# Performance work log

Measured on AMD Instinct MI355X. Metric: run time of the kernel, lower is better.

## Reference

```python
import jax, jax.numpy as jnp
import numpy as np

N_GROUPS = 32  # getGroupSize(.) assumed -> channels // 8 (or //24 for 3*ch) == 32 for ch=256
HEADS = 4


def group_norm(x, gamma, beta, groups=N_GROUPS, eps=1e-5):
    n, c = x.shape
    xg = x.reshape(n, groups, c // groups)
    mu = xg.mean(-1, keepdims=True)
    var = xg.var(-1, keepdims=True)
    xn = ((xg - mu) * jax.lax.rsqrt(var + eps)).reshape(n, c)
    return xn * gamma + beta


def setup_inputs():
    key = jax.random.key(0)
    N, E, CH, HID = 2000, 16000, 256, 256
    ks = jax.random.split(key, 24)

    def w(k, shape, s=0.02):
        return (jax.random.normal(k, shape) * s).astype(jnp.float32)

    inp = {
        'x': jax.random.normal(ks[0], (N, CH), jnp.float32),
        'edge_index': jax.random.randint(ks[1], (2, E), 0, N),
        'edge_attr': jax.random.normal(ks[2], (E, CH), jnp.float32),
        # edge_mlp: GN(3ch)+ReLU -> Linear(3ch,hid) -> GN(hid)+ReLU -> Linear(hid,ch)
        'gn_e1_g': jnp.ones((3 * CH,), jnp.float32), 'gn_e1_b': jnp.zeros((3 * CH,), jnp.float32),
        'We1': w(ks[3], (3 * CH, HID)), 'be1': jnp.zeros((HID,), jnp.float32),
        'gn_e2_g': jnp.ones((HID,), jnp.float32), 'gn_e2_b': jnp.zeros((HID,), jnp.float32),
        'We2': w(ks[4], (HID, CH)), 'be2': jnp.zeros((CH,), jnp.float32),
        # actN: GN(ch)+ReLU
        'gn_n_g': jnp.ones((CH,), jnp.float32), 'gn_n_b': jnp.zeros((CH,), jnp.float32),
        # multi-head attention projections
        'Wq': w(ks[5], (CH, CH)), 'bq': jnp.zeros((CH,), jnp.float32),
        'Wk': w(ks[6], (CH, CH)), 'bk': jnp.zeros((CH,), jnp.float32),
        'Wv': w(ks[7], (CH, CH)), 'bv': jnp.zeros((CH,), jnp.float32),
        'Wo': w(ks[8], (CH, CH)), 'bo': jnp.zeros((CH,), jnp.float32),
        # node_mlp: Linear(2ch,hid) -> GN(hid)+ReLU -> Linear(hid,ch)
        'Wn1': w(ks[9], (2 * CH, HID)), 'bn1': jnp.zeros((HID,), jnp.float32),
        'gn_n2_g': jnp.ones((HID,), jnp.float32), 'gn_n2_b': jnp.zeros((HID,), jnp.float32),
        'Wn2': w(ks[10], (HID, CH)), 'bn2': jnp.zeros((CH,), jnp.float32),
    }
    return inp


def reference(x, edge_index, edge_attr,
              gn_e1_g, gn_e1_b, We1, be1, gn_e2_g, gn_e2_b, We2, be2,
              gn_n_g, gn_n_b, Wq, bq, Wk, bk, Wv, bv, Wo, bo,
              Wn1, bn1, gn_n2_g, gn_n2_b, Wn2, bn2):
    row, col = edge_index[0], edge_index[1]
    N, ch = x.shape
    E = edge_attr.shape[0]
    dk = ch // HEADS

    # ---- edge model: cat(src, tgt, e) -> GN/ReLU -> Lin -> GN/ReLU -> Lin (+res) ----
    e_in = jnp.concatenate([x[row], x[col], edge_attr], axis=1)  # [E, 3ch]
    h = jax.nn.relu(group_norm(e_in, gn_e1_g, gn_e1_b))
    h = h @ We1 + be1
    h = jax.nn.relu(group_norm(h, gn_e2_g, gn_e2_b))
    e_out = h @ We2 + be2 + edge_attr  # [E, ch]

    # ---- node model: dense-masked MHA, queries=nodes, keys/values=edges ----
    mask = jnp.zeros((N, E), x.dtype).at[col, jnp.arange(E)].set(1.0)  # scatter adjacency
    q = (x @ Wq + bq).reshape(N, HEADS, dk)
    k = (e_out @ Wk + bk).reshape(E, HEADS, dk)
    v = (e_out @ Wv + bv).reshape(E, HEADS, dk)
    scores = jnp.einsum('nhd,ehd->hne', q, k) / jnp.sqrt(jnp.float32(dk))  # [H, N, E]
    scores = jnp.where(mask[None] > 0, scores, jnp.float32(-1e9))
    attn = jax.nn.softmax(scores, axis=-1)
    g = jnp.einsum('hne,ehd->nhd', attn, v).reshape(N, ch) @ Wo + bo  # [N, ch]

    xa = jax.nn.relu(group_norm(x, gn_n_g, gn_n_b))
    h = jnp.concatenate([xa, g], axis=1) @ Wn1 + bn1  # thinker='cat'
    h = jax.nn.relu(group_norm(h, gn_n2_g, gn_n2_b))
    n_out = h @ Wn2 + bn2 + x  # residual

    return n_out, e_out
```

## Files before the change

kernel.cpp:

```cpp
#include <hip/hip_runtime.h>
#include <hip/hip_bf16.h>
#include <stdint.h>
#include <math.h>

#define CH 256

typedef __attribute__((ext_vector_type(8)))  short short8;
typedef __attribute__((ext_vector_type(16))) short short16;
typedef __attribute__((ext_vector_type(4)))  float f32x4;

#define GL2LDS16(g, l) __builtin_amdgcn_global_load_lds(                       \
    (const __attribute__((address_space(1))) void*)(g),                        \
    (__attribute__((address_space(3))) void*)(l), 16, 0, 0)

__device__ inline short f2bf(float f) {
    __hip_bfloat16 h = __float2bfloat16(f);
    short s;
    __builtin_memcpy(&s, &h, 2);
    return s;
}

__device__ inline float bf2f(short s) {
    unsigned u = ((unsigned)(unsigned short)s) << 16;
    float f;
    __builtin_memcpy(&f, &u, 4);
    return f;
}

__device__ inline float warp_sum64(float v) {
    v += __shfl_xor(v, 32, 64);
    v += __shfl_xor(v, 16, 64);
    v += __shfl_xor(v, 8, 64);
    v += __shfl_xor(v, 4, 64);
    v += __shfl_xor(v, 2, 64);
    v += __shfl_xor(v, 1, 64);
    return v;
}

__device__ inline float warp_max64(float v) {
    v = fmaxf(v, __shfl_xor(v, 32, 64));
    v = fmaxf(v, __shfl_xor(v, 16, 64));
    v = fmaxf(v, __shfl_xor(v, 8, 64));
    v = fmaxf(v, __shfl_xor(v, 4, 64));
    v = fmaxf(v, __shfl_xor(v, 2, 64));
    v = fmaxf(v, __shfl_xor(v, 1, 64));
    return v;
}

struct GArgs {
    const short* A; const short* Bt; const float* bias; const float* res;
    float* C; short* Cbf;
    const float* gamma; const float* beta; float* vbar;
    int M, K, Nc, ldc, coff;
    const short* A2; const short* Bt2; const float* bias2; short* Cbf2;
    int M2, Nc2, y_split;
    const short* xbf; const short* eabf; const int* rowi; const int* coli;
    const float* mu; const float* rs; const float* vg; const float* vbt;
    int* cursor; int* elist;
};

template <int BM, int BN, int AMODE, int EPI, int DUAL, int VB, int FILL>
__global__ __launch_bounds__(256) void mfma_gemm(GArgs g)
{
    constexpr int BK = 64;
    constexpr int AK = AMODE ? (BK + 8) : BK;
    constexpr int HM = BM / 2, HN = BN / 2;
    constexpr int FM = HM / 16, FN = HN / 16;
    constexpr int PA = BM / 32;
    constexpr int PB = BN / 32;
    __shared__ short As[BM * AK];
    __shared__ short Bs[BN * BK];
    __shared__ int sidx[AMODE ? 2 * BM : 1];

    const short* A = g.A; const short* Bt = g.Bt;
    const float* bias = g.bias; const float* res = g.res;
    float* C = g.C; short* Cbf = g.Cbf;
    int M = g.M, ldc = g.ldc, co = g.coff;
    const int K = g.K;
    int by = blockIdx.y, bx = blockIdx.x;
    bool qrole = false;
    if constexpr (DUAL) {
        if (by >= g.y_split) {
            by -= g.y_split;
            if (bx * BN >= g.Nc2) return;
            qrole = true;
            A = g.A2; Bt = g.Bt2; bias = g.bias2; Cbf = g.Cbf2;
            C = nullptr; res = nullptr;
            M = g.M2; ldc = g.Nc2; co = 0;
        }
    }

    const int t = threadIdx.x;
    const int wave = t >> 6, lane = t & 63;
    const int q = lane >> 4, l16 = lane & 15;
    const int row0 = by * BM;
    const int col0 = bx * BN;
    const int wm = wave & 1, wn = wave >> 1;

    if constexpr (AMODE) {
        if (t < BM) {
            int gr = row0 + t; if (gr >= M) gr = M - 1;
            sidx[t] = g.rowi[gr];
            sidx[BM + t] = g.coli[gr];
        }
        __syncthreads();
    }

    if constexpr (FILL) {
        if (!qrole && bx == 0 && t < BM) {
            int rg = row0 + t;
            if (rg < M) {
                int c = g.coli[rg];
                int p = atomicAdd(&g.cursor[c], 1);
                g.elist[p] = rg;
            }
        }
    }

    f32x4 acc[FM][FN];
    #pragma unroll
    for (int i = 0; i < FM; i++)
        #pragma unroll
        for (int j = 0; j < FN; j++) acc[i][j] = (f32x4){0.f, 0.f, 0.f, 0.f};

    for (int k0 = 0; k0 < K; k0 += BK) {
        if constexpr (AMODE == 1) {
            int reg = k0 >> 8;
            int rloc = t >> 3;
            int c8 = (t & 7) * 8;
            int pos = k0 + c8;
            int G = pos / 24;
            float4 ga  = *(const float4*)&g.vg[pos];
            float4 ga2 = *(const float4*)&g.vg[pos + 4];
            float4 gb  = *(const float4*)&g.vbt[pos];
            float4 gb2 = *(const float4*)&g.vbt[pos + 4];
            int off = pos & 255;
            #pragma unroll
            for (int p = 0; p < BM / 32; p++) {
                int r2 = p * 32 + rloc;
                int e = row0 + r2; if (e >= M) e = M - 1;
                const short* srow;
                if (reg == 0)      srow = g.xbf + (size_t)sidx[r2] * CH;
                else if (reg == 1) srow = g.xbf + (size_t)sidx[BM + r2] * CH;
                else               srow = g.eabf + (size_t)e * CH;
                short8 v8 = *(const short8*)&srow[off];
                float mm = g.mu[(size_t)e * 32 + G];
                float rr = g.rs[(size_t)e * 32 + G];
                short8 o;
                o[0] = f2bf(fmaxf((bf2f(v8[0]) - mm) * rr * ga.x + gb.x, 0.f));
                o[1] = f2bf(fmaxf((bf2f(v8[1]) - mm) * rr * ga.y + gb.y, 0.f));
                o[2] = f2bf(fmaxf((bf2f(v8[2]) - mm) * rr * ga.z + gb.z, 0.f));
                o[3] = f2bf(fmaxf((bf2f(v8[3]) - mm) * rr * ga.w + gb.w, 0.f));
                o[4] = f2bf(fmaxf((bf2f(v8[4]) - mm) * rr * ga2.x + gb2.x, 0.f));
                o[5] = f2bf(fmaxf((bf2f(v8[5]) - mm) * rr * ga2.y + gb2.y, 0.f));
                o[6] = f2bf(fmaxf((bf2f(v8[6]) - mm) * rr * ga2.z + gb2.z, 0.f));
                o[7] = f2bf(fmaxf((bf2f(v8[7]) - mm) * rr * ga2.w + gb2.w, 0.f));
                *(short8*)&As[r2 * AK + c8] = o;
            }
        } else {
            #pragma unroll
            for (int p = 0; p < PA; p++) {
                int chunk = p * 256 + t;
                int r = chunk >> 3;
                int cs = (((chunk & 7) ^ (r & 7)) * 8);
                int gr = row0 + r; if (gr >= M) gr = M - 1;
                const short* gsrc = A + (size_t)gr * K + k0 + cs;
                short* ldst = &As[(p * 256 + wave * 64) * 8];
                GL2LDS16(gsrc, ldst);
            }
        }
        #pragma unroll
        for (int p = 0; p < PB; p++) {
            int chunk = p * 256 + t;
            int r = chunk >> 3;
            int cs = (((chunk & 7) ^ (r & 7)) * 8);
            const short* gsrc = Bt + (size_t)(col0 + r) * K + k0 + cs;
            short* ldst = &Bs[(p * 256 + wave * 64) * 8];
            GL2LDS16(gsrc, ldst);
        }
        __syncthreads();
        #pragma unroll
        for (int ks = 0; ks < 2; ks++) {
            short8 af[FM], bf[FN];
            #pragma unroll
            for (int mi = 0; mi < FM; mi++) {
                int R = wm * HM + mi * 16 + l16;
                if constexpr (AMODE == 1)
                    af[mi] = *(const short8*)&As[R * AK + ks * 32 + q * 8];
                else {
                    int slot = ((ks * 4 + q) ^ (R & 7)) * 8;
                    af[mi] = *(const short8*)&As[R * BK + slot];
                }
            }
            #pragma unroll
            for (int ni = 0; ni < FN; ni++) {
                int R = wn * HN + ni * 16 + l16;
                int slot = ((ks * 4 + q) ^ (R & 7)) * 8;
                bf[ni] = *(const short8*)&Bs[R * BK + slot];
            }
            #pragma unroll
            for (int mi = 0; mi < FM; mi++)
                #pragma unroll
                for (int ni = 0; ni < FN; ni++)
                    acc[mi][ni] = __builtin_amdgcn_mfma_f32_16x16x32_bf16(
                        af[mi], bf[ni], acc[mi][ni], 0, 0, 0);
        }
        __syncthreads();
    }

    #pragma unroll
    for (int ni = 0; ni < FN; ni++) {
        int cg = col0 + wn * HN + ni * 16 + l16;
        float bv = bias[cg];
        if constexpr (EPI == 1) {
            float ga = g.gamma[cg], be = g.beta[cg];
            #pragma unroll
            for (int mi = 0; mi < FM; mi++) {
                #pragma unroll
                for (int r = 0; r < 4; r++) {
                    float v = acc[mi][ni][r] + bv;
                    float s = v, sq = v * v;
                    s += __shfl_xor(s, 1, 64);  sq += __shfl_xor(sq, 1, 64);
                    s += __shfl_xor(s, 2, 64);  sq += __shfl_xor(sq, 2, 64);
                    s += __shfl_xor(s, 4, 64);  sq += __shfl_xor(sq, 4, 64);
                    float mean = s * 0.125f;
                    float var = sq * 0.125f - mean * mean;
                    float o = fmaxf((v - mean) * rsqrtf(var + 1e-5f) * ga + be, 0.f);
                    int rg = row0 + wm * HM + mi * 16 + q * 4 + r;
                    if (rg < M) Cbf[(size_t)rg * ldc + co + cg] = f2bf(o);
                }
            }
        } else {
            #pragma unroll
            for (int mi = 0; mi < FM; mi++) {
                #pragma unroll
                for (int r = 0; r < 4; r++) {
                    int rg = row0 + wm * HM + mi * 16 + q * 4 + r;
                    if (rg < M) {
                        float v = acc[mi][ni][r] + bv;
                        if (res) v += res[(size_t)rg * ldc + co + cg];
                        if (C)   C[(size_t)rg * ldc + co + cg] = v;
                        if (Cbf) Cbf[(size_t)rg * ldc + co + cg] = f2bf(v);
                    }
                }
            }
            if constexpr (VB) {
                if (!qrole && cg >= 256) {
                    float part = 0.f;
                    #pragma unroll
                    for (int mi = 0; mi < FM; mi++)
                        #pragma unroll
                        for (int r = 0; r < 4; r++) {
                            int rg = row0 + wm * HM + mi * 16 + q * 4 + r;
                            if (rg < M) part += acc[mi][ni][r] + bv;
                        }
                    part += __shfl_xor(part, 16, 64);
                    part += __shfl_xor(part, 32, 64);
                    if (q == 0) atomicAdd(&g.vbar[cg - 256], part);
                }
            }
        }
    }
}

struct PrepPack {
    const float* wsrc[8];
    short* wdst[8];
    int wK[8];
    int wstart[8];
    int NW, NP;
    const float* x;
    short* x_bf;
    short* cat_bf;
    float2* xs;
    const float* gng;
    const float* gnb;
    float* vbar;
    const float* bk;
    const float* bv;
    float* bkv;
    int* counts;
    int N;
};

__global__ __launch_bounds__(256) void prep_kernel(PrepPack p)
{
    int bid = blockIdx.x;
    int t = threadIdx.x;
    if (bid < p.NW) {
        int m = 0;
        #pragma unroll
        for (int i = 1; i < 8; i++) if (bid >= p.wstart[i]) m = i;
        int k0 = (bid - p.wstart[m]) * 16;
        const float* src = p.wsrc[m];
        short16 o;
        #pragma unroll
        for (int j = 0; j < 16; j++) o[j] = f2bf(src[(size_t)(k0 + j) * 256 + t]);
        *(short16*)(p.wdst[m] + (size_t)t * p.wK[m] + k0) = o;
        return;
    }
    if (bid >= p.NW + p.NP) {
        int i = (bid - p.NW - p.NP) * 256 + t;
        if (i < p.N) p.counts[i] = 0;
        return;
    }
    int pb = bid - p.NW;
    if (pb == 0) {
        p.vbar[t] = 0.f;
        p.bkv[t] = p.bk[t];
        p.bkv[256 + t] = p.bv[t];
    }
    int r = pb * 8 + (t >> 5);
    int g = t & 31;
    if (r >= p.N) return;
    size_t xb = (size_t)r * CH + g * 8;
    float4 a = *(const float4*)&p.x[xb];
    float4 b = *(const float4*)&p.x[xb + 4];
    short8 xr;
    xr[0] = f2bf(a.x); xr[1] = f2bf(a.y); xr[2] = f2bf(a.z); xr[3] = f2bf(a.w);
    xr[4] = f2bf(b.x); xr[5] = f2bf(b.y); xr[6] = f2bf(b.z); xr[7] = f2bf(b.w);
    *(short8*)&p.x_bf[xb] = xr;
    float s  = a.x + a.y + a.z + a.w + b.x + b.y + b.z + b.w;
    float s2 = a.x*a.x + a.y*a.y + a.z*a.z + a.w*a.w
             + b.x*b.x + b.y*b.y + b.z*b.z + b.w*b.w;
    p.xs[(size_t)r * 32 + g] = make_float2(s, s2);
    float m = s * 0.125f;
    float var = s2 * 0.125f - m * m;
    float rsd = rsqrtf(var + 1e-5f);
    float4 g0 = *(const float4*)&p.gng[g * 8];
    float4 g1 = *(const float4*)&p.gng[g * 8 + 4];
    float4 b0 = *(const float4*)&p.gnb[g * 8];
    float4 b1 = *(const float4*)&p.gnb[g * 8 + 4];
    short8 o;
    o[0] = f2bf(fmaxf((a.x - m) * rsd * g0.x + b0.x, 0.f));
    o[1] = f2bf(fmaxf((a.y - m) * rsd * g0.y + b0.y, 0.f));
    o[2] = f2bf(fmaxf((a.z - m) * rsd * g0.z + b0.z, 0.f));
    o[3] = f2bf(fmaxf((a.w - m) * rsd * g0.w + b0.w, 0.f));
    o[4] = f2bf(fmaxf((b.x - m) * rsd * g1.x + b1.x, 0.f));
    o[5] = f2bf(fmaxf((b.y - m) * rsd * g1.y + b1.y, 0.f));
    o[6] = f2bf(fmaxf((b.z - m) * rsd * g1.z + b1.z, 0.f));
    o[7] = f2bf(fmaxf((b.w - m) * rsd * g1.w + b1.w, 0.f));
    *(short8*)&p.cat_bf[(size_t)r * (2 * CH) + g * 8] = o;
}

__global__ __launch_bounds__(256) void estats_kernel(
    const float* __restrict__ eattr, const int* __restrict__ rowi,
    const int* __restrict__ coli, const float2* __restrict__ xs,
    float* __restrict__ mu, float* __restrict__ rs,
    short* __restrict__ eabf, int* __restrict__ counts, int E)
{
    __shared__ float2 ea[8][32];
    int t = threadIdx.x;
    int slot = t >> 5, g = t & 31;
    int e = blockIdx.x * 8 + slot;
    float4 a = *(const float4*)&eattr[(size_t)e * CH + g * 8];
    float4 b = *(const float4*)&eattr[(size_t)e * CH + g * 8 + 4];
    short8 o8;
    o8[0] = f2bf(a.x); o8[1] = f2bf(a.y); o8[2] = f2bf(a.z); o8[3] = f2bf(a.w);
    o8[4] = f2bf(b.x); o8[5] = f2bf(b.y); o8[6] = f2bf(b.z); o8[7] = f2bf(b.w);
    *(short8*)&eabf[(size_t)e * CH + g * 8] = o8;
    float s  = a.x + a.y + a.z + a.w + b.x + b.y + b.z + b.w;
    float s2 = a.x*a.x + a.y*a.y + a.z*a.z + a.w*a.w
             + b.x*b.x + b.y*b.y + b.z*b.z + b.w*b.w;
    ea[slot][g] = make_float2(s, s2);
    int r = rowi[e], c = coli[e];
    if (g == 0) atomicAdd(&counts[c], 1);
    __syncthreads();
    float S = 0.f, S2 = 0.f;
    #pragma unroll
    for (int j = 0; j < 3; j++) {
        int b3 = 3 * g + j;
        int src = b3 >> 5, idx = b3 & 31;
        float2 v;
        if (src == 0)      v = xs[(size_t)r * 32 + idx];
        else if (src == 1) v = xs[(size_t)c * 32 + idx];
        else               v = ea[slot][idx];
        S += v.x; S2 += v.y;
    }
    float m = S * (1.f / 24.f);
    float var = S2 * (1.f / 24.f) - m * m;
    mu[(size_t)e * 32 + g] = m;
    rs[(size_t)e * 32 + g] = rsqrtf(var + 1e-5f);
}

__global__ __launch_bounds__(1024) void scan_kernel(
    const int* __restrict__ counts, int* __restrict__ offsets,
    int* __restrict__ cursor, int N)
{
    __shared__ int s[1024];
    int t = threadIdx.x;
    int a = (2 * t     < N) ? counts[2 * t]     : 0;
    int b = (2 * t + 1 < N) ? counts[2 * t + 1] : 0;
    s[t] = a + b;
    __syncthreads();
    for (int off = 1; off < 1024; off <<= 1) {
        int v = (t >= off) ? s[t - off] : 0;
        __syncthreads();
        s[t] += v;
        __syncthreads();
    }
    int excl = (t > 0) ? s[t - 1] : 0;
    if (2 * t < N)     { offsets[2 * t]     = excl;     cursor[2 * t]     = excl; }
    if (2 * t + 1 < N) { offsets[2 * t + 1] = excl + a; cursor[2 * t + 1] = excl + a; }
    if (t == 1023) offsets[N] = s[1023];
}

__global__ __launch_bounds__(256) void attn_kernel(
    const short* __restrict__ qb, const short* __restrict__ kvb,
    const int* __restrict__ offsets, const int* __restrict__ elist,
    const float* __restrict__ vbar, short* __restrict__ g_bf, int N, int E)
{
    __shared__ int eidx[64];
    __shared__ float scl[4 * 64];
    int n = blockIdx.x;
    int wave = threadIdx.x >> 6;
    int lane = threadIdx.x & 63;
    int s0 = offsets[n], s1 = offsets[n + 1];
    float q0 = bf2f(qb[(size_t)n * CH + lane]);
    float q1 = bf2f(qb[(size_t)n * CH + 64 + lane]);
    float q2 = bf2f(qb[(size_t)n * CH + 128 + lane]);
    float q3 = bf2f(qb[(size_t)n * CH + 192 + lane]);
    float out = 0.f, m = -INFINITY, l = 0.f;
    for (int base = s0; base < s1; base += 64) {
        int cn = s1 - base; if (cn > 64) cn = 64;
        if (wave == 0 && lane < cn) eidx[lane] = elist[base + lane];
        __syncthreads();
        for (int j = wave; j < cn; j += 4) {
            int e = eidx[j];
            const short* kr = kvb + (size_t)e * 512;
            float d0 = warp_sum64(q0 * bf2f(kr[lane]));
            float d1 = warp_sum64(q1 * bf2f(kr[64 + lane]));
            float d2 = warp_sum64(q2 * bf2f(kr[128 + lane]));
            float d3 = warp_sum64(q3 * bf2f(kr[192 + lane]));
            if (lane == 0) {
                scl[j]       = d0 * 0.125f;
                scl[64 + j]  = d1 * 0.125f;
                scl[128 + j] = d2 * 0.125f;
                scl[192 + j] = d3 * 0.125f;
            }
        }
        __syncthreads();
        float s = (lane < cn) ? scl[wave * 64 + lane] : -INFINITY;
        float mc = warp_max64(s);
        float nm = fmaxf(m, mc);
        float scale = __expf(m - nm);
        float pp = (lane < cn) ? __expf(s - nm) : 0.f;
        float ps = warp_sum64(pp);
        l = l * scale + ps;
        out *= scale;
        m = nm;
        for (int i = 0; i < cn; i++) {
            float pi = __shfl(pp, i, 64);
            int ei = eidx[i];
            out += pi * bf2f(kvb[(size_t)ei * 512 + 256 + wave * 64 + lane]);
        }
        __syncthreads();
    }
    float res;
    if (s1 > s0) res = out / l;
    else         res = vbar[wave * 64 + lane] * (1.f / (float)E);
    g_bf[(size_t)n * CH + wave * 64 + lane] = f2bf(res);
}

extern "C" void kernel_launch(void* const* d_in, const int* in_sizes, int n_in,
                              void* d_out, int out_size, void* d_ws, size_t ws_size,
                              hipStream_t stream)
{
    const float* x       = (const float*)d_in[0];
    const int*   ei      = (const int*)d_in[1];
    const float* eattr   = (const float*)d_in[2];
    const float* gn_e1_g = (const float*)d_in[3];
    const float* gn_e1_b = (const float*)d_in[4];
    const float* We1     = (const float*)d_in[5];
    const float* be1     = (const float*)d_in[6];
    const float* gn_e2_g = (const float*)d_in[7];
    const float* gn_e2_b = (const float*)d_in[8];
    const float* We2     = (const float*)d_in[9];
    const float* be2     = (const float*)d_in[10];
    const float* gn_n_g  = (const float*)d_in[11];
    const float* gn_n_b  = (const float*)d_in[12];
    const float* Wq      = (const float*)d_in[13];
    const float* bq      = (const float*)d_in[14];
    const float* Wk      = (const float*)d_in[15];
    const float* bk      = (const float*)d_in[16];
    const float* Wv      = (const float*)d_in[17];
    const float* bv      = (const float*)d_in[18];
    const float* Wo      = (const float*)d_in[19];
    const float* bo      = (const float*)d_in[20];
    const float* Wn1     = (const float*)d_in[21];
    const float* bn1     = (const float*)d_in[22];
    const float* gn_n2_g = (const float*)d_in[23];
    const float* gn_n2_b = (const float*)d_in[24];
    const float* Wn2     = (const float*)d_in[25];
    const float* bn2     = (const float*)d_in[26];

    const int N = in_sizes[0] / CH;
    const int E = in_sizes[2] / CH;

    float* nout = (float*)d_out;
    float* eout = (float*)d_out + (size_t)N * CH;

    char* base = (char*)d_ws;
    short* kv_bf  = (short*)base; base += (size_t)E * 512 * 2;
    short* h2_bf  = (short*)base; base += (size_t)E * CH * 2;
    short* eo_bf  = (short*)base; base += (size_t)E * CH * 2;
    short* eabf   = (short*)base; base += (size_t)E * CH * 2;
    short* q_bf   = (short*)base; base += (size_t)N * CH * 2;
    short* g_bf   = (short*)base; base += (size_t)N * CH * 2;
    short* cat_bf = (short*)base; base += (size_t)N * 2 * CH * 2;
    short* hn_bf  = (short*)base; base += (size_t)N * CH * 2;
    short* x_bf   = (short*)base; base += (size_t)N * CH * 2;
    float2* xs    = (float2*)base; base += (size_t)N * 32 * 8;
    float* mub    = (float*)base; base += (size_t)E * 32 * 4;
    float* rsb    = (float*)base; base += (size_t)E * 32 * 4;
    float* vbar   = (float*)base; base += 1024;
    float* bkv    = (float*)base; base += 2048;
    short* We1t = (short*)base; base += (size_t)768 * 256 * 2;
    short* We2t = (short*)base; base += (size_t)256 * 256 * 2;
    short* Wqt  = (short*)base; base += (size_t)256 * 256 * 2;
    short* Wkvt = (short*)base; base += (size_t)512 * 256 * 2;
    short* Wot  = (short*)base; base += (size_t)256 * 256 * 2;
    short* Wn1t = (short*)base; base += (size_t)512 * 256 * 2;
    short* Wn2t = (short*)base; base += (size_t)256 * 256 * 2;
    int* counts  = (int*)base;
    int* offsets = counts + N;
    int* cursor  = offsets + (N + 1) + 3;
    int* elist   = cursor + N;

    const int* rowi = ei;
    const int* coli = ei + E;

    dim3 blk(256);

    PrepPack pp;
    const float* wsrc[8] = {We1, We2, Wq, Wk, Wv, Wo, Wn1, Wn2};
    short* wdst[8] = {We1t, We2t, Wqt, Wkvt, Wkvt + (size_t)256 * 256, Wot, Wn1t, Wn2t};
    const int wKd[8] = {768, 256, 256, 256, 256, 256, 512, 256};
    int acc = 0;
    for (int i = 0; i < 8; i++) {
        pp.wsrc[i] = wsrc[i]; pp.wdst[i] = wdst[i]; pp.wK[i] = wKd[i];
        pp.wstart[i] = acc; acc += wKd[i] / 16;
    }
    pp.NW = acc;
    pp.NP = (N + 7) / 8;
    pp.x = x; pp.x_bf = x_bf; pp.cat_bf = cat_bf; pp.xs = xs;
    pp.gng = gn_n_g; pp.gnb = gn_n_b;
    pp.vbar = vbar; pp.bk = bk; pp.bv = bv; pp.bkv = bkv;
    pp.counts = counts; pp.N = N;
    int nzero = (N + 255) / 256;
    prep_kernel<<<pp.NW + pp.NP + nzero, blk, 0, stream>>>(pp);

    estats_kernel<<<E / 8, blk, 0, stream>>>(eattr, rowi, coli, xs, mub, rsb,
                                             eabf, counts, E);
    scan_kernel<<<1, 1024, 0, stream>>>(counts, offsets, cursor, N);

    GArgs ga = {};
    ga.Bt = We1t; ga.bias = be1; ga.Cbf = h2_bf;
    ga.gamma = gn_e2_g; ga.beta = gn_e2_b;
    ga.M = E; ga.K = 3 * CH; ga.Nc = CH; ga.ldc = CH; ga.coff = 0;
    ga.xbf = x_bf; ga.eabf = eabf; ga.rowi = rowi; ga.coli = coli;
    ga.mu = mub; ga.rs = rsb; ga.vg = gn_e1_g; ga.vbt = gn_e1_b;
    mfma_gemm<64, 64, 1, 1, 0, 0, 0><<<dim3(4, E / 64), blk, 0, stream>>>(ga);

    ga = {};
    ga.A = h2_bf; ga.Bt = We2t; ga.bias = be2; ga.res = eattr;
    ga.C = eout; ga.Cbf = eo_bf;
    ga.M = E; ga.K = CH; ga.Nc = CH; ga.ldc = CH; ga.coff = 0;
    mfma_gemm<64, 64, 0, 0, 0, 0, 0><<<dim3(4, E / 64), blk, 0, stream>>>(ga);

    ga = {};
    ga.A = eo_bf; ga.Bt = Wkvt; ga.bias = bkv; ga.Cbf = kv_bf; ga.vbar = vbar;
    ga.M = E; ga.K = CH; ga.Nc = 512; ga.ldc = 512; ga.coff = 0;
    ga.A2 = x_bf; ga.Bt2 = Wqt; ga.bias2 = bq; ga.Cbf2 = q_bf;
    ga.M2 = N; ga.Nc2 = CH; ga.y_split = E / 64;
    ga.coli = coli; ga.cursor = cursor; ga.elist = elist;
    mfma_gemm<64, 64, 0, 0, 1, 1, 1><<<dim3(8, E / 64 + (N + 63) / 64), blk, 0, stream>>>(ga);

    attn_kernel<<<N, blk, 0, stream>>>(q_bf, kv_bf, offsets, elist, vbar, g_bf, N, E);

    ga = {};
    ga.A = g_bf; ga.Bt = Wot; ga.bias = bo; ga.Cbf = cat_bf;
    ga.M = N; ga.K = CH; ga.Nc = CH; ga.ldc = 2 * CH; ga.coff = CH;
    mfma_gemm<32, 64, 0, 0, 0, 0, 0><<<dim3(4, (N + 31) / 32), blk, 0, stream>>>(ga);

    ga = {};
    ga.A = cat_bf; ga.Bt = Wn1t; ga.bias = bn1; ga.Cbf = hn_bf;
    ga.gamma = gn_n2_g; ga.beta = gn_n2_b;
    ga.M = N; ga.K = 2 * CH; ga.Nc = CH; ga.ldc = CH; ga.coff = 0;
    mfma_gemm<32, 64, 0, 1, 0, 0, 0><<<dim3(4, (N + 31) / 32), blk, 0, stream>>>(ga);

    ga = {};
    ga.A = hn_bf; ga.Bt = Wn2t; ga.bias = bn2; ga.res = x; ga.C = nout;
    ga.M = N; ga.K = CH; ga.Nc = CH; ga.ldc = CH; ga.coff = 0;
    mfma_gemm<32, 64, 0, 0, 0, 0, 0><<<dim3(4, (N + 31) / 32), blk, 0, stream>>>(ga);
}
```

Baseline: 240.2 us.

## Fuse node-side Wo, Wn1+GroupNorm, Wn2 GEMMs into one tail kernel

Replaces three separate node-model GEMM launches (output projection, node MLP first layer with GroupNorm+ReLU, second layer with residual) with a single kernel. Each block handles 32 rows across the full 256-column width and keeps intermediates in LDS instead of writing them to global memory. This removes two launches and the global round trips of g-projection and hidden activations. In exchange the grid drops to about 63 blocks instead of 4x that per GEMM, which lowers parallelism on a large GPU.

After: 249.3 us. +3.8%, slower.

```diff
diff --git a/kernel.cpp b/kernel.cpp
--- a/kernel.cpp
+++ b/kernel.cpp
@@ -257,6 +257,163 @@
                     part += __shfl_xor(part, 16, 64);
                     part += __shfl_xor(part, 32, 64);
                     if (q == 0) atomicAdd(&g.vbar[cg - 256], part);
+                }
+            }
+        }
+    }
+}
+
+struct TailArgs {
+    const short* gbf;
+    const short* catbf;
+    const short* Wot;
+    const short* Wn1t;
+    const short* Wn2t;
+    const float* bo; const float* bn1; const float* bn2;
+    const float* g2; const float* b2;
+    const float* x; float* nout;
+    int M;
+};
+
+__global__ __launch_bounds__(256) void tail_kernel(TailArgs a)
+{
+    constexpr int BK = 64;
+    __shared__ short Bs[256 * BK];
+    __shared__ short As[32 * BK];
+    __shared__ short H[32 * 256];
+    const int t = threadIdx.x;
+    const int wave = t >> 6, lane = t & 63;
+    const int q = lane >> 4, l16 = lane & 15;
+    const int row0 = blockIdx.x * 32;
+    const int M = a.M;
+
+    f32x4 acc[2][4];
+
+    auto zero_acc = [&]() {
+        #pragma unroll
+        for (int i = 0; i < 2; i++)
+            #pragma unroll
+            for (int j = 0; j < 4; j++) acc[i][j] = (f32x4){0.f, 0.f, 0.f, 0.f};
+    };
+    auto stageB = [&](const short* Bt, int K, int k0) {
+        #pragma unroll
+        for (int p = 0; p < 8; p++) {
+            int chunk = p * 256 + t;
+            int r = chunk >> 3;
+            int cs = (((chunk & 7) ^ (r & 7)) * 8);
+            const short* gsrc = Bt + (size_t)r * K + k0 + cs;
+            short* ldst = &Bs[(p * 256 + wave * 64) * 8];
+            GL2LDS16(gsrc, ldst);
+        }
+    };
+    auto stageA = [&](const short* A, int lda, int k0) {
+        int r = t >> 3;
+        int cs = (((t & 7) ^ (r & 7)) * 8);
+        int gr = row0 + r; if (gr >= M) gr = M - 1;
+        const short* gsrc = A + (size_t)gr * lda + k0 + cs;
+        short* ldst = &As[(wave * 64) * 8];
+        GL2LDS16(gsrc, ldst);
+    };
+    auto compute = [&](int w, int src) {
+        #pragma unroll
+        for (int ks = 0; ks < 2; ks++) {
+            short8 af[2], bf[4];
+            #pragma unroll
+            for (int mi = 0; mi < 2; mi++) {
+                int R = mi * 16 + l16;
+                int slot = ((ks * 4 + q) ^ (R & 7)) * 8;
+                if (src == 0) af[mi] = *(const short8*)&As[R * BK + slot];
+                else          af[mi] = *(const short8*)&H[R * 256 + w * 64 + slot];
+            }
+            #pragma unroll
+            for (int ni = 0; ni < 4; ni++) {
+                int R = wave * 64 + ni * 16 + l16;
+                int slot = ((ks * 4 + q) ^ (R & 7)) * 8;
+                bf[ni] = *(const short8*)&Bs[R * BK + slot];
+            }
+            #pragma unroll
+            for (int mi = 0; mi < 2; mi++)
+                #pragma unroll
+                for (int ni = 0; ni < 4; ni++)
+                    acc[mi][ni] = __builtin_amdgcn_mfma_f32_16x16x32_bf16(
+                        af[mi], bf[ni], acc[mi][ni], 0, 0, 0);
+        }
+    };
+    auto hwrite = [&](int R, int cg, float v) {
+        int cl = cg & 63;
+        int c = cl >> 3, o = cl & 7;
+        H[R * 256 + (cg & ~63) + ((c ^ (R & 7)) << 3) + o] = f2bf(v);
+    };
+
+    zero_acc();
+    for (int k0 = 0; k0 < 256; k0 += BK) {
+        stageA(a.gbf, 256, k0);
+        stageB(a.Wot, 256, k0);
+        __syncthreads();
+        compute(0, 0);
+        __syncthreads();
+    }
+    #pragma unroll
+    for (int ni = 0; ni < 4; ni++) {
+        int cg = wave * 64 + ni * 16 + l16;
+        float bv = a.bo[cg];
+        #pragma unroll
+        for (int mi = 0; mi < 2; mi++)
+            #pragma unroll
+            for (int r = 0; r < 4; r++)
+                hwrite(mi * 16 + q * 4 + r, cg, acc[mi][ni][r] + bv);
+    }
+
+    zero_acc();
+    for (int k0 = 0; k0 < 512; k0 += BK) {
+        int src = (k0 < 256) ? 0 : 1;
+        if (src == 0) stageA(a.catbf, 512, k0);
+        stageB(a.Wn1t, 512, k0);
+        __syncthreads();
+        compute((k0 - 256) >> 6, src);
+        __syncthreads();
+    }
+    #pragma unroll
+    for (int ni = 0; ni < 4; ni++) {
+        int cg = wave * 64 + ni * 16 + l16;
+        float bv = a.bn1[cg];
+        float ga = a.g2[cg], be = a.b2[cg];
+        #pragma unroll
+        for (int mi = 0; mi < 2; mi++) {
+            #pragma unroll
+            for (int r = 0; r < 4; r++) {
+                float v = acc[mi][ni][r] + bv;
+                float s = v, sq = v * v;
+                s += __shfl_xor(s, 1, 64);  sq += __shfl_xor(sq, 1, 64);
+                s += __shfl_xor(s, 2, 64);  sq += __shfl_xor(sq, 2, 64);
+                s += __shfl_xor(s, 4, 64);  sq += __shfl_xor(sq, 4, 64);
+                float mean = s * 0.125f;
+                float var = sq * 0.125f - mean * mean;
+                float o = fmaxf((v - mean) * rsqrtf(var + 1e-5f) * ga + be, 0.f);
+                hwrite(mi * 16 + q * 4 + r, cg, o);
+            }
+        }
+    }
+
+    zero_acc();
+    for (int k0 = 0; k0 < 256; k0 += BK) {
+        stageB(a.Wn2t, 256, k0);
+        __syncthreads();
+        compute(k0 >> 6, 1);
+        __syncthreads();
+    }
+    #pragma unroll
+    for (int ni = 0; ni < 4; ni++) {
+        int cg = wave * 64 + ni * 16 + l16;
+        float bv = a.bn2[cg];
+        #pragma unroll
+        for (int mi = 0; mi < 2; mi++) {
+            #pragma unroll
+            for (int r = 0; r < 4; r++) {
+                int rg = row0 + mi * 16 + q * 4 + r;
+                if (rg < M) {
+                    float v = acc[mi][ni][r] + bv + a.x[(size_t)rg * 256 + cg];
+                    a.nout[(size_t)rg * 256 + cg] = v;
                 }
             }
         }
@@ -529,6 +686,7 @@
 
     const int* rowi = ei;
     const int* coli = ei + E;
+    (void)hn_bf;
 
     dim3 blk(256);
 
@@ -578,19 +736,12 @@
 
     attn_kernel<<<N, blk, 0, stream>>>(q_bf, kv_bf, offsets, elist, vbar, g_bf, N, E);
 
-    ga = {};
-    ga.A = g_bf; ga.Bt = Wot; ga.bias = bo; ga.Cbf = cat_bf;
-    ga.M = N; ga.K = CH; ga.Nc = CH; ga.ldc = 2 * CH; ga.coff = CH;
-    mfma_gemm<32, 64, 0, 0, 0, 0, 0><<<dim3(4, (N + 31) / 32), blk, 0, stream>>>(ga);
-
-    ga = {};
-    ga.A = cat_bf; ga.Bt = Wn1t; ga.bias = bn1; ga.Cbf = hn_bf;
-    ga.gamma = gn_n2_g; ga.beta = gn_n2_b;
-    ga.M = N; ga.K = 2 * CH; ga.Nc = CH; ga.ldc = CH; ga.coff = 0;
-    mfma_gemm<32, 64, 0, 1, 0, 0, 0><<<dim3(4, (N + 31) / 32), blk, 0, stream>>>(ga);
-
-    ga = {};
-    ga.A = hn_bf; ga.Bt = Wn2t; ga.bias = bn2; ga.res = x; ga.C = nout;
-    ga.M = N; ga.K = CH; ga.Nc = CH; ga.ldc = CH; ga.coff = 0;
-    mfma_gemm<32, 64, 0, 0, 0, 0, 0><<<dim3(4, (N + 31) / 32), blk, 0, stream>>>(ga);
-}
+    TailArgs ta;
+    ta.gbf = g_bf; ta.catbf = cat_bf;
+    ta.Wot = Wot; ta.Wn1t = Wn1t; ta.Wn2t = Wn2t;
+    ta.bo = bo; ta.bn1 = bn1; ta.bn2 = bn2;
+    ta.g2 = gn_n2_g; ta.b2 = gn_n2_b;
+    ta.x = x; ta.nout = nout;
+    ta.M = N;
+    tail_kernel<<<(N + 31) / 32, blk, 0, stream>>>(ta);
+}
```

## Fold offsets scan into edge GEMM grid and pair K/V panels per block

Applied to the files above, without the earlier changes.

Removes the standalone scan kernel and runs the counts prefix-scan in an extra row of blocks appended to the first edge GEMM launch, saving one launch. The KV projection GEMM now computes the K and V column panels (256 apart) in the same block, reusing the loaded A tile for both and halving the grid's x-dimension. Query-role blocks skip the second panel. The trade-offs are doubled accumulator registers and B-tile LDS, and a single scan block that may finish after the GEMM blocks.

New measurement: 238.1 us. No clear change (-0.9%).

```diff
diff --git a/kernel.cpp b/kernel.cpp
--- a/kernel.cpp
+++ b/kernel.cpp
@@ -57,9 +57,11 @@
     const short* xbf; const short* eabf; const int* rowi; const int* coli;
     const float* mu; const float* rs; const float* vg; const float* vbt;
     int* cursor; int* elist;
+    const int* counts; int* offsets; int Nn;
 };
 
-template <int BM, int BN, int AMODE, int EPI, int DUAL, int VB, int FILL>
+template <int BM, int BN, int AMODE, int EPI, int DUAL, int VB, int FILL,
+          int SCAN = 0, int PAN2 = 0>
 __global__ __launch_bounds__(256) void mfma_gemm(GArgs g)
 {
     constexpr int BK = 64;
@@ -68,8 +70,9 @@
     constexpr int FM = HM / 16, FN = HN / 16;
     constexpr int PA = BM / 32;
     constexpr int PB = BN / 32;
+    constexpr int NP2 = PAN2 ? 2 : 1;
     __shared__ short As[BM * AK];
-    __shared__ short Bs[BN * BK];
+    __shared__ short Bs[NP2 * BN * BK];
     __shared__ int sidx[AMODE ? 2 * BM : 1];
 
     const short* A = g.A; const short* Bt = g.Bt;
@@ -78,6 +81,44 @@
     int M = g.M, ldc = g.ldc, co = g.coff;
     const int K = g.K;
     int by = blockIdx.y, bx = blockIdx.x;
+
+    if constexpr (SCAN) {
+        if (by == (int)gridDim.y - 1) {
+            const int t0 = threadIdx.x;
+            if (bx == 0) {
+                int* ss = (int*)As;
+                int base8 = t0 * 8;
+                int loc[8]; int srun = 0;
+                #pragma unroll
+                for (int j = 0; j < 8; j++) {
+                    int idx = base8 + j;
+                    int c = (idx < g.Nn) ? g.counts[idx] : 0;
+                    loc[j] = srun; srun += c;
+                }
+                ss[t0] = srun;
+                __syncthreads();
+                for (int off = 1; off < 256; off <<= 1) {
+                    int v = (t0 >= off) ? ss[t0 - off] : 0;
+                    __syncthreads();
+                    ss[t0] += v;
+                    __syncthreads();
+                }
+                int excl = (t0 > 0) ? ss[t0 - 1] : 0;
+                #pragma unroll
+                for (int j = 0; j < 8; j++) {
+                    int idx = base8 + j;
+                    if (idx < g.Nn) {
+                        int v = excl + loc[j];
+                        g.offsets[idx] = v;
+                        g.cursor[idx]  = v;
+                    }
+                }
+                if (t0 == 255) g.offsets[g.Nn] = ss[255];
+            }
+            return;
+        }
+    }
+
     bool qrole = false;
     if constexpr (DUAL) {
         if (by >= g.y_split) {
@@ -117,11 +158,13 @@
         }
     }
 
-    f32x4 acc[FM][FN];
+    f32x4 acc[NP2][FM][FN];
     #pragma unroll
-    for (int i = 0; i < FM; i++)
+    for (int p2 = 0; p2 < NP2; p2++)
         #pragma unroll
-        for (int j = 0; j < FN; j++) acc[i][j] = (f32x4){0.f, 0.f, 0.f, 0.f};
+        for (int i = 0; i < FM; i++)
+            #pragma unroll
+            for (int j = 0; j < FN; j++) acc[p2][i][j] = (f32x4){0.f, 0.f, 0.f, 0.f};
 
     for (int k0 = 0; k0 < K; k0 += BK) {
         if constexpr (AMODE == 1) {
@@ -170,18 +213,23 @@
             }
         }
         #pragma unroll
-        for (int p = 0; p < PB; p++) {
-            int chunk = p * 256 + t;
-            int r = chunk >> 3;
-            int cs = (((chunk & 7) ^ (r & 7)) * 8);
-            const short* gsrc = Bt + (size_t)(col0 + r) * K + k0 + cs;
-            short* ldst = &Bs[(p * 256 + wave * 64) * 8];
-            GL2LDS16(gsrc, ldst);
+        for (int p2 = 0; p2 < NP2; p2++) {
+            if (!(PAN2 && p2 == 1 && qrole)) {
+                #pragma unroll
+                for (int p = 0; p < PB; p++) {
+                    int chunk = p * 256 + t;
+                    int r = chunk >> 3;
+                    int cs = (((chunk & 7) ^ (r & 7)) * 8);
+                    const short* gsrc = Bt + (size_t)(col0 + p2 * 256 + r) * K + k0 + cs;
+                    short* ldst = &Bs[p2 * BN * BK + (p * 256 + wave * 64) * 8];
+                    GL2LDS16(gsrc, ldst);
+                }
+            }
         }
         __syncthreads();
         #pragma unroll
         for (int ks = 0; ks < 2; ks++) {
-            short8 af[FM], bf[FN];
+            short8 af[FM];
             #pragma unroll
             for (int mi = 0; mi < FM; mi++) {
                 int R = wm * HM + mi * 16 + l16;
@@ -193,70 +241,81 @@
                 }
             }
             #pragma unroll
-            for (int ni = 0; ni < FN; ni++) {
-                int R = wn * HN + ni * 16 + l16;
-                int slot = ((ks * 4 + q) ^ (R & 7)) * 8;
-                bf[ni] = *(const short8*)&Bs[R * BK + slot];
-            }
-            #pragma unroll
-            for (int mi = 0; mi < FM; mi++)
-                #pragma unroll
-                for (int ni = 0; ni < FN; ni++)
-                    acc[mi][ni] = __builtin_amdgcn_mfma_f32_16x16x32_bf16(
-                        af[mi], bf[ni], acc[mi][ni], 0, 0, 0);
-        }
-        __syncthreads();
-    }
-
-    #pragma unroll
-    for (int ni = 0; ni < FN; ni++) {
-        int cg = col0 + wn * HN + ni * 16 + l16;
-        float bv = bias[cg];
-        if constexpr (EPI == 1) {
-            float ga = g.gamma[cg], be = g.beta[cg];
-            #pragma unroll
-            for (int mi = 0; mi < FM; mi++) {
-                #pragma unroll
-                for (int r = 0; r < 4; r++) {
-                    float v = acc[mi][ni][r] + bv;
-                    float s = v, sq = v * v;
-                    s += __shfl_xor(s, 1, 64);  sq += __shfl_xor(sq, 1, 64);
-                    s += __shfl_xor(s, 2, 64);  sq += __shfl_xor(sq, 2, 64);
-                    s += __shfl_xor(s, 4, 64);  sq += __shfl_xor(sq, 4, 64);
-                    float mean = s * 0.125f;
-                    float var = sq * 0.125f - mean * mean;
-                    float o = fmaxf((v - mean) * rsqrtf(var + 1e-5f) * ga + be, 0.f);
-                    int rg = row0 + wm * HM + mi * 16 + q * 4 + r;
-                    if (rg < M) Cbf[(size_t)rg * ldc + co + cg] = f2bf(o);
-                }
-            }
-        } else {
-            #pragma unroll
-            for (int mi = 0; mi < FM; mi++) {
-                #pragma unroll
-                for (int r = 0; r < 4; r++) {
-                    int rg = row0 + wm * HM + mi * 16 + q * 4 + r;
-                    if (rg < M) {
-                        float v = acc[mi][ni][r] + bv;
-                        if (res) v += res[(size_t)rg * ldc + co + cg];
-                        if (C)   C[(size_t)rg * ldc + co + cg] = v;
-                        if (Cbf) Cbf[(size_t)rg * ldc + co + cg] = f2bf(v);
+            for (int p2 = 0; p2 < NP2; p2++) {
+                if (!(PAN2 && p2 == 1 && qrole)) {
+                    short8 bfr[FN];
+                    #pragma unroll
+                    for (int ni = 0; ni < FN; ni++) {
+                        int R = wn * HN + ni * 16 + l16;
+                        int slot = ((ks * 4 + q) ^ (R & 7)) * 8;
+                        bfr[ni] = *(const short8*)&Bs[p2 * BN * BK + R * BK + slot];
                     }
-                }
-            }
-            if constexpr (VB) {
-                if (!qrole && cg >= 256) {
-                    float part = 0.f;
                     #pragma unroll
                     for (int mi = 0; mi < FM; mi++)
                         #pragma unroll
-                        for (int r = 0; r < 4; r++) {
-                            int rg = row0 + wm * HM + mi * 16 + q * 4 + r;
-                            if (rg < M) part += acc[mi][ni][r] + bv;
+                        for (int ni = 0; ni < FN; ni++)
+                            acc[p2][mi][ni] = __builtin_amdgcn_mfma_f32_16x16x32_bf16(
+                                af[mi], bfr[ni], acc[p2][mi][ni], 0, 0, 0);
+                }
+            }
+        }
+        __syncthreads();
+    }
+
+    #pragma unroll
+    for (int p2 = 0; p2 < NP2; p2++) {
+        if (PAN2 && p2 == 1 && qrole) continue;
+        #pragma unroll
+        for (int ni = 0; ni < FN; ni++) {
+            int cg = col0 + p2 * 256 + wn * HN + ni * 16 + l16;
+            float bv = bias[cg];
+            if constexpr (EPI == 1) {
+                float ga = g.gamma[cg], be = g.beta[cg];
+                #pragma unroll
+                for (int mi = 0; mi < FM; mi++) {
+                    #pragma unroll
+                    for (int r = 0; r < 4; r++) {
+                        float v = acc[p2][mi][ni][r] + bv;
+                        float s = v, sq = v * v;
+                        s += __shfl_xor(s, 1, 64);  sq += __shfl_xor(sq, 1, 64);
+                        s += __shfl_xor(s, 2, 64);  sq += __shfl_xor(sq, 2, 64);
+                        s += __shfl_xor(s, 4, 64);  sq += __shfl_xor(sq, 4, 64);
+                        float mean = s * 0.125f;
+                        float var = sq * 0.125f - mean * mean;
+                        float o = fmaxf((v - mean) * rsqrtf(var + 1e-5f) * ga + be, 0.f);
+                        int rg = row0 + wm * HM + mi * 16 + q * 4 + r;
+                        if (rg < M) Cbf[(size_t)rg * ldc + co + cg] = f2bf(o);
+                    }
+                }
+            } else {
+                #pragma unroll
+                for (int mi = 0; mi < FM; mi++) {
+                    #pragma unroll
+                    for (int r = 0; r < 4; r++) {
+                        int rg = row0 + wm * HM + mi * 16 + q * 4 + r;
+                        if (rg < M) {
+                            float v = acc[p2][mi][ni][r] + bv;
+                            if (res) v += res[(size_t)rg * ldc + co + cg];
+                            if (C)   C[(size_t)rg * ldc + co + cg] = v;
+                            if (Cbf) Cbf[(size_t)rg * ldc + co + cg] = f2bf(v);
                         }
-                    part += __shfl_xor(part, 16, 64);
-                    part += __shfl_xor(part, 32, 64);
-                    if (q == 0) atomicAdd(&g.vbar[cg - 256], part);
+                    }
+                }
+                if constexpr (VB) {
+                    bool vpanel = PAN2 ? (p2 == 1) : (!qrole && cg >= 256);
+                    if (vpanel) {
+                        float part = 0.f;
+                        #pragma unroll
+                        for (int mi = 0; mi < FM; mi++)
+                            #pragma unroll
+                            for (int r = 0; r < 4; r++) {
+                                int rg = row0 + wm * HM + mi * 16 + q * 4 + r;
+                                if (rg < M) part += acc[p2][mi][ni][r] + bv;
+                            }
+                        part += __shfl_xor(part, 16, 64);
+                        part += __shfl_xor(part, 32, 64);
+                        if (q == 0) atomicAdd(&g.vbar[cg - 256], part);
+                    }
                 }
             }
         }
@@ -383,28 +442,6 @@
     rs[(size_t)e * 32 + g] = rsqrtf(var + 1e-5f);
 }
 
-__global__ __launch_bounds__(1024) void scan_kernel(
-    const int* __restrict__ counts, int* __restrict__ offsets,
-    int* __restrict__ cursor, int N)
-{
-    __shared__ int s[1024];
-    int t = threadIdx.x;
-    int a = (2 * t     < N) ? counts[2 * t]     : 0;
-    int b = (2 * t + 1 < N) ? counts[2 * t + 1] : 0;
-    s[t] = a + b;
-    __syncthreads();
-    for (int off = 1; off < 1024; off <<= 1) {
-        int v = (t >= off) ? s[t - off] : 0;
-        __syncthreads();
-        s[t] += v;
-        __syncthreads();
-    }
-    int excl = (t > 0) ? s[t - 1] : 0;
-    if (2 * t < N)     { offsets[2 * t]     = excl;     cursor[2 * t]     = excl; }
-    if (2 * t + 1 < N) { offsets[2 * t + 1] = excl + a; cursor[2 * t + 1] = excl + a; }
-    if (t == 1023) offsets[N] = s[1023];
-}
-
 __global__ __launch_bounds__(256) void attn_kernel(
     const short* __restrict__ qb, const short* __restrict__ kvb,
     const int* __restrict__ offsets, const int* __restrict__ elist,
@@ -552,7 +589,6 @@
 
     estats_kernel<<<E / 8, blk, 0, stream>>>(eattr, rowi, coli, xs, mub, rsb,
                                              eabf, counts, E);
-    scan_kernel<<<1, 1024, 0, stream>>>(counts, offsets, cursor, N);
 
     GArgs ga = {};
     ga.Bt = We1t; ga.bias = be1; ga.Cbf = h2_bf;
@@ -560,7 +596,8 @@
     ga.M = E; ga.K = 3 * CH; ga.Nc = CH; ga.ldc = CH; ga.coff = 0;
     ga.xbf = x_bf; ga.eabf = eabf; ga.rowi = rowi; ga.coli = coli;
     ga.mu = mub; ga.rs = rsb; ga.vg = gn_e1_g; ga.vbt = gn_e1_b;
-    mfma_gemm<64, 64, 1, 1, 0, 0, 0><<<dim3(4, E / 64), blk, 0, stream>>>(ga);
+    ga.counts = counts; ga.offsets = offsets; ga.cursor = cursor; ga.Nn = N;
+    mfma_gemm<64, 64, 1, 1, 0, 0, 0, 1, 0><<<dim3(4, E / 64 + 1), blk, 0, stream>>>(ga);
 
     ga = {};
     ga.A = h2_bf; ga.Bt = We2t; ga.bias = be2; ga.res = eattr;
@@ -574,7 +611,7 @@
     ga.A2 = x_bf; ga.Bt2 = Wqt; ga.bias2 = bq; ga.Cbf2 = q_bf;
     ga.M2 = N; ga.Nc2 = CH; ga.y_split = E / 64;
     ga.coli = coli; ga.cursor = cursor; ga.elist = elist;
-    mfma_gemm<64, 64, 0, 0, 1, 1, 1><<<dim3(8, E / 64 + (N + 63) / 64), blk, 0, stream>>>(ga);
+    mfma_gemm<64, 64, 0, 0, 1, 1, 1, 0, 1><<<dim3(4, E / 64 + (N + 63) / 64), blk, 0, stream>>>(ga);
 
     attn_kernel<<<N, blk, 0, stream>>>(q_bf, kv_bf, offsets, elist, vbar, g_bf, N, E);
 
```
